# Kernel tuning notes

Measured on AMD Instinct MI355X. Metric: run time of the kernel, lower is better.

The kernel has to match this reference:

```python
import jax, jax.numpy as jnp
import numpy as np

B, N, D, H = 2, 1024, 512, 16
DH = D // H  # d_head = 32
NEG_INF = -1e9
LN_EPS = 1e-5


def setup_inputs() -> dict:
    key = jax.random.key(0)
    ks = jax.random.split(key, 12)
    x = jax.random.normal(ks[0], (B, N, D), dtype=jnp.float32)
    pdist = jax.random.uniform(ks[1], (B, N, N), dtype=jnp.float32)
    angle = jax.random.normal(ks[2], (B, N, N, 2), dtype=jnp.float32)
    adj = jax.random.uniform(ks[3], (B, N, N), dtype=jnp.float32)
    mask = jnp.zeros((B, 1, 1, N), dtype=bool)
    # parameters
    gamma_p = jnp.ones((H,), dtype=jnp.float32)
    gamma_adj = jnp.ones((H,), dtype=jnp.float32)
    w_bias = jax.random.normal(ks[4], (H, 2), dtype=jnp.float32) / np.sqrt(2.0)   # Linear(2,H).weight
    att_w = jax.random.normal(ks[5], (3 * H * DH, D), dtype=jnp.float32) / np.sqrt(D)  # Linear(D,3HDh).weight
    ff_w = jax.random.normal(ks[6], (D, H * DH), dtype=jnp.float32) / np.sqrt(H * DH)  # Linear(HDh,D).weight
    ff_b = jnp.zeros((D,), dtype=jnp.float32)
    ln_w = jnp.ones((D,), dtype=jnp.float32)
    ln_b = jnp.zeros((D,), dtype=jnp.float32)
    return dict(x=x, pdist=pdist, angle=angle, adj=adj, mask=mask,
                gamma_p=gamma_p, gamma_adj=gamma_adj, w_bias=w_bias,
                att_w=att_w, ff_w=ff_w, ff_b=ff_b, ln_w=ln_w, ln_b=ln_b)


def reference(x, pdist, angle, adj, mask, gamma_p, gamma_adj, w_bias,
              att_w, ff_w, ff_b, ln_w, ln_b):
    bsz, n_atoms, _ = x.shape
    # QKV projection
    qkv = x @ att_w.T                              # [B,N,3*H*DH]
    wq, wk, wv = jnp.split(qkv, 3, axis=-1)
    wq = wq.reshape(bsz, n_atoms, H, DH)
    wk = wk.reshape(bsz, n_atoms, H, DH)
    wv = wv.reshape(bsz, n_atoms, H, DH)
    # scores with additive biases
    score = jnp.einsum('bihd,bjhd->bhij', wq, wk) / jnp.sqrt(jnp.float32(DH))
    score = score - gamma_p[None, :, None, None] * pdist[:, None]
    angle_bias = jnp.einsum('bijc,hc->bhij', angle, w_bias)
    score = score + angle_bias
    score = score + gamma_adj[None, :, None, None] * adj[:, None]
    score = jnp.where(mask, NEG_INF, score)
    prob = jax.nn.softmax(score, axis=-1)          # [B,H,N,N]
    att_vec = jnp.einsum('bhij,bjhd->bihd', prob, wv).reshape(bsz, n_atoms, H * DH)
    ff_out = att_vec @ ff_w.T + ff_b               # [B,N,D]
    y = x + ff_out
    mu = jnp.mean(y, axis=-1, keepdims=True)
    var = jnp.mean(jnp.square(y - mu), axis=-1, keepdims=True)
    return (y - mu) / jnp.sqrt(var + LN_EPS) * ln_w + ln_b
```

## Files before the change

### kernel.cpp

```cpp
#include <hip/hip_runtime.h>
#include <hip/hip_bf16.h>
#include <stdint.h>

#define DEVI __device__ __forceinline__

typedef __attribute__((ext_vector_type(4))) float f32x4;
typedef __attribute__((ext_vector_type(16))) float f32x16;
typedef __attribute__((ext_vector_type(8))) short bf16x8;

constexpr int nB = 2, nN = 1024, nD = 512, nH = 16, nDH = 32;

DEVI unsigned short f2bf(float x) {
  unsigned u = __float_as_uint(x);
  return (unsigned short)((u + 0x7fffu + ((u >> 16) & 1u)) >> 16);
}
DEVI float bf2f(unsigned short s) { return __uint_as_float(((unsigned)s) << 16); }
DEVI unsigned pk2(float lo, float hi_) {
  return (unsigned)f2bf(lo) | ((unsigned)f2bf(hi_) << 16);
}
DEVI float bperm(int srclane, float v) {
  return __int_as_float(__builtin_amdgcn_ds_bpermute(srclane << 2, __float_as_int(v)));
}
DEVI void gload16(const void* g, void* l) {
  __builtin_amdgcn_global_load_lds((const __attribute__((address_space(1))) void*)g,
                                   (__attribute__((address_space(3))) void*)l, 16, 0, 0);
}

__global__ __launch_bounds__(256) void cvt_kernel(const float* __restrict__ x,
                                                  const float* __restrict__ aw,
                                                  const float* __restrict__ fw,
                                                  unsigned short* __restrict__ xb,
                                                  unsigned short* __restrict__ awb,
                                                  unsigned short* __restrict__ fwb) {
  int i = blockIdx.x * 256 + threadIdx.x;
  const float* src; unsigned short* dst; int base;
  if (i < 262144)      { src = x;  dst = xb;  base = i; }
  else if (i < 458752) { src = aw; dst = awb; base = i - 262144; }
  else                 { src = fw; dst = fwb; base = i - 458752; }
  float4 v = reinterpret_cast<const float4*>(src)[base];
  ushort4 o;
  o.x = f2bf(v.x); o.y = f2bf(v.y); o.z = f2bf(v.z); o.w = f2bf(v.w);
  reinterpret_cast<ushort4*>(dst)[base] = o;
}

template <int BM, int BN, int MODE>
__global__ __launch_bounds__(256, 4) void gemm_bt(const unsigned short* __restrict__ A,
                                                  const unsigned short* __restrict__ Bw,
                                                  unsigned short* __restrict__ q,
                                                  unsigned short* __restrict__ kmat,
                                                  unsigned short* __restrict__ vm,
                                                  float* __restrict__ C,
                                                  int K, int Ncols) {
  constexpr int MW = BM / 2, NW = BN / 2;
  constexpr int MF = MW / 16, NF = NW / 16;
  constexpr int IA = BM / 16, IB = BN / 16, PW = (IA + IB) / 4;
  __shared__ __align__(16) unsigned short sA[2][BM * 32];
  __shared__ __align__(16) unsigned short sB[2][BN * 32];
  const int tid = threadIdx.x, wid = tid >> 6, lane = tid & 63;
  const int wr = wid >> 1, wc = wid & 1;
  const long rowA = (long)blockIdx.x * BM;
  const long rowB = (long)blockIdx.y * BN;
  const int srow = lane >> 2, scol = (lane & 3) * 8;

  f32x4 acc[MF][NF];
#pragma unroll
  for (int mm = 0; mm < MF; ++mm)
#pragma unroll
    for (int nn = 0; nn < NF; ++nn)
#pragma unroll
      for (int r = 0; r < 4; ++r) acc[mm][nn][r] = 0.f;

  auto stage = [&](int t, int pb) {
    const int k0 = t * 32;
#pragma unroll
    for (int j = 0; j < PW; ++j) {
      int g = wid + 4 * j;
      if (g < IA) {
        gload16(&A[(rowA + g * 16 + srow) * K + k0 + scol], &sA[pb][g * 512]);
      } else {
        int c = g - IA;
        gload16(&Bw[(rowB + c * 16 + srow) * K + k0 + scol], &sB[pb][c * 512]);
      }
    }
  };
  auto comp = [&](int pb) {
    const int kg = (lane >> 4) * 8, rlo = lane & 15;
    bf16x8 af[MF], bfv[NF];
#pragma unroll
    for (int mm = 0; mm < MF; ++mm)
      af[mm] = *reinterpret_cast<const bf16x8*>(&sA[pb][(MW * wr + 16 * mm + rlo) * 32 + kg]);
#pragma unroll
    for (int nn = 0; nn < NF; ++nn)
      bfv[nn] = *reinterpret_cast<const bf16x8*>(&sB[pb][(NW * wc + 16 * nn + rlo) * 32 + kg]);
#pragma unroll
    for (int mm = 0; mm < MF; ++mm)
#pragma unroll
      for (int nn = 0; nn < NF; ++nn)
        acc[mm][nn] = __builtin_amdgcn_mfma_f32_16x16x32_bf16(af[mm], bfv[nn],
                                                              acc[mm][nn], 0, 0, 0);
  };

  const int NT = K / 32;
  stage(0, 0);
  __syncthreads();
  for (int t = 0; t < NT; t += 2) {
    if (t + 1 < NT) stage(t + 1, 1);
    comp(0);
    __syncthreads();
    if (t + 2 < NT) stage(t + 2, 0);
    if (t + 1 < NT) comp(1);
    __syncthreads();
  }

#pragma unroll
  for (int mm = 0; mm < MF; ++mm)
#pragma unroll
    for (int nn = 0; nn < NF; ++nn)
#pragma unroll
      for (int r = 0; r < 4; ++r) {
        float v = acc[mm][nn][r];
        int row = (int)rowA + MW * wr + 16 * mm + (lane >> 4) * 4 + r;
        int col = (int)rowB + NW * wc + 16 * nn + (lane & 15);
        if constexpr (MODE == 0) {
          int s = col >> 9, rem = col & 511;
          int h = rem >> 5, d = rem & 31;
          int b = row >> 10, n = row & 1023;
          long idx = ((long)(b * nH + h) * nN + n) * nDH + d;
          if (s == 0)      q[idx]    = f2bf(v * 0.1767766952966369f);
          else if (s == 1) kmat[idx] = f2bf(v);
          else             vm[idx]   = f2bf(v);
        } else {
          C[(long)row * Ncols + col] = v;
        }
      }
}

__global__ __launch_bounds__(256) void vtrans_kernel(const unsigned short* __restrict__ vm,
                                                     unsigned short* __restrict__ vtt) {
  const int g = blockIdx.x, bh = g >> 3, oct = g & 7;
  const int t = threadIdx.x;
  __shared__ unsigned short tile[32][36];
  for (int s = 0; s < 4; ++s) {
    const int jt = oct * 4 + s;
    {
      int r = t >> 3, c4 = (t & 7) * 4;
      *reinterpret_cast<ushort4*>(&tile[r][c4]) = *reinterpret_cast<const ushort4*>(
          vm + ((long)bh * nN + jt * 32 + r) * 32 + c4);
    }
    __syncthreads();
    {
      int d = t >> 3, j4 = (t & 7) * 4;
      ushort4 o;
      o.x = tile[j4][d]; o.y = tile[j4 + 1][d];
      o.z = tile[j4 + 2][d]; o.w = tile[j4 + 3][d];
      *reinterpret_cast<ushort4*>(vtt + ((long)bh * 32 + jt) * 1024 + d * 32 + j4) = o;
    }
    __syncthreads();
  }
}

__global__ __launch_bounds__(1024, 4) void attn_kernel(
    const unsigned short* __restrict__ qm, const unsigned short* __restrict__ km,
    const unsigned short* __restrict__ vtt,
    const float* __restrict__ pdist, const float* __restrict__ angle,
    const float* __restrict__ adj, const unsigned char* __restrict__ mask,
    const float* __restrict__ gamma_p, const float* __restrict__ gamma_adj,
    const float* __restrict__ w_bias,
    unsigned short* __restrict__ po, float* __restrict__ pm, float* __restrict__ pl) {
  const int b = blockIdx.x >> 5, it = blockIdx.x & 31;
  const int jc = blockIdx.y;
  const int tid = threadIdx.x, wid = tid >> 6, lane = tid & 63;
  const int h = wid;
  const int li = lane & 31, hi = lane >> 5;
  const int ibase = it * 32;

  __shared__ __align__(16) float s_pd[2][1024], s_adj[2][1024];
  __shared__ __align__(16) float s_a0[2][1024], s_a1[2][1024];
  __shared__ __align__(16) float s_mk[1024];

  const float gp = gamma_p[h], ga = gamma_adj[h];
  const float wb0 = w_bias[2 * h], wb1 = w_bias[2 * h + 1];

  const unsigned short* qb = qm + ((long)(b * nH + h) * nN + ibase) * nDH;
  const bf16x8 qf0 = *reinterpret_cast<const bf16x8*>(qb + li * 32 + hi * 8);
  const bf16x8 qf1 = *reinterpret_cast<const bf16x8*>(qb + li * 32 + 16 + hi * 8);

  f32x16 o;
#pragma unroll
  for (int r = 0; r < 16; ++r) o[r] = 0.f;
  float mrun = -INFINITY, lrun = 0.f;

  auto stage = [&](int s, int pb) {
    const int jbase = (jc * 8 + s) * 32;
    if (tid < 512) {
      int r = (tid >> 3) & 31, c = tid & 7;
      const float* src = (tid < 256 ? pdist : adj) +
                         ((long)b * nN + ibase + r) * nN + jbase + c * 4;
      float4 v = *reinterpret_cast<const float4*>(src);
      float* dst = (tid < 256 ? s_pd[pb] : s_adj[pb]) + r * 32 + ((c ^ (r & 7)) << 2);
      *reinterpret_cast<float4*>(dst) = v;
    } else {
      int t2 = tid - 512;
      int r = t2 >> 4, p = t2 & 15;
      float4 v = *reinterpret_cast<const float4*>(
          angle + (((long)b * nN + ibase + r) * nN + jbase + p * 2) * 2);
      int off = r * 32 + (((p >> 1) ^ (r & 7)) << 2) + (p & 1) * 2;
      *reinterpret_cast<float2*>(s_a0[pb] + off) = make_float2(v.x, v.z);
      *reinterpret_cast<float2*>(s_a1[pb] + off) = make_float2(v.y, v.w);
    }
  };

  auto comp = [&](int s, int pb) {
    const int jt = jc * 8 + s, jbase = jt * 32;
    const unsigned short* kb = km + ((long)(b * nH + h) * nN + jbase) * nDH;
    bf16x8 kf0 = *reinterpret_cast<const bf16x8*>(kb + li * 32 + hi * 8);
    bf16x8 kf1 = *reinterpret_cast<const bf16x8*>(kb + li * 32 + 16 + hi * 8);
    f32x16 sc;
#pragma unroll
    for (int r = 0; r < 16; ++r) sc[r] = 0.f;
    sc = __builtin_amdgcn_mfma_f32_32x32x16_bf16(kf0, qf0, sc, 0, 0, 0);
    sc = __builtin_amdgcn_mfma_f32_32x32x16_bf16(kf1, qf1, sc, 0, 0, 0);

    float sv[16];
    float tmax = -INFINITY;
#pragma unroll
    for (int g = 0; g < 4; ++g) {
      const int cs = (((2 * g + hi) ^ (li & 7)) << 2);
      f32x4 pdq = *reinterpret_cast<const f32x4*>(s_pd[pb] + li * 32 + cs);
      f32x4 adq = *reinterpret_cast<const f32x4*>(s_adj[pb] + li * 32 + cs);
      f32x4 a0q = *reinterpret_cast<const f32x4*>(s_a0[pb] + li * 32 + cs);
      f32x4 a1q = *reinterpret_cast<const f32x4*>(s_a1[pb] + li * 32 + cs);
      f32x4 mkq = *reinterpret_cast<const f32x4*>(s_mk + jbase + 8 * g + 4 * hi);
#pragma unroll
      for (int u = 0; u < 4; ++u) {
        float x = sc[4 * g + u] - gp * pdq[u] + wb0 * a0q[u] + wb1 * a1q[u]
                  + ga * adq[u] + mkq[u];
        sv[4 * g + u] = x;
        tmax = fmaxf(tmax, x);
      }
    }
    tmax = fmaxf(tmax, __shfl_xor(tmax, 32));
    if (__any((int)(tmax > mrun + 8.f))) {
      float mnew = fmaxf(mrun, tmax);
      float alpha = __expf(mrun - mnew);
      lrun *= alpha;
#pragma unroll
      for (int r = 0; r < 16; ++r) o[r] *= bperm((r & 3) + 8 * (r >> 2) + 4 * hi, alpha);
      mrun = mnew;
    }
    float psum = 0.f;
#pragma unroll
    for (int r = 0; r < 16; ++r) { sv[r] = __expf(sv[r] - mrun); psum += sv[r]; }
    psum += __shfl_xor(psum, 32);
    lrun += psum;

    unsigned ow[8], rw[8];
#pragma unroll
    for (int t = 0; t < 8; ++t) ow[t] = pk2(sv[2 * t], sv[2 * t + 1]);
#pragma unroll
    for (int t = 0; t < 8; ++t) rw[t] = __shfl_xor(ow[t], 32);
    union U { unsigned u[4]; bf16x8 v; };
    U u0, u1;
    if (hi == 0) {
      u0.u[0] = ow[0]; u0.u[1] = ow[1]; u0.u[2] = rw[0]; u0.u[3] = rw[1];
      u1.u[0] = ow[4]; u1.u[1] = ow[5]; u1.u[2] = rw[4]; u1.u[3] = rw[5];
    } else {
      u0.u[0] = rw[2]; u0.u[1] = rw[3]; u0.u[2] = ow[2]; u0.u[3] = ow[3];
      u1.u[0] = rw[6]; u1.u[1] = rw[7]; u1.u[2] = ow[6]; u1.u[3] = ow[7];
    }

    const unsigned short* vb = vtt + ((long)(b * nH + h) * 32 + jt) * 1024;
    bf16x8 vf0 = *reinterpret_cast<const bf16x8*>(vb + li * 32 + hi * 8);
    bf16x8 vf1 = *reinterpret_cast<const bf16x8*>(vb + li * 32 + 16 + hi * 8);
    o = __builtin_amdgcn_mfma_f32_32x32x16_bf16(u0.v, vf0, o, 0, 0, 0);
    o = __builtin_amdgcn_mfma_f32_32x32x16_bf16(u1.v, vf1, o, 0, 0, 0);
  };

  s_mk[tid] = mask[b * nN + tid] ? -1e9f : 0.f;
  stage(0, 0);
  __syncthreads();
  for (int s = 0; s < 8; s += 2) {
    if (s + 1 < 8) stage(s + 1, 1);
    comp(s, 0);
    __syncthreads();
    if (s + 2 < 8) stage(s + 2, 0);
    comp(s + 1, 1);
    __syncthreads();
  }

  const long task = (((long)(b * nH + h) * 32 + it) * 4 + jc);
  unsigned short* pob = po + task * 1024;
#pragma unroll
  for (int r = 0; r < 16; ++r) {
    const int irow = (r & 3) + 8 * (r >> 2) + 4 * hi;
    pob[irow * 32 + li] = f2bf(o[r]);
  }
  if (hi == 0) { pm[task * 32 + li] = mrun; pl[task * 32 + li] = lrun; }
}

__global__ __launch_bounds__(256) void merge_kernel(const unsigned short* __restrict__ po,
                                                    const float* __restrict__ pm,
                                                    const float* __restrict__ pl,
                                                    unsigned short* __restrict__ attb) {
  const int x = blockIdx.x;
  const int t = threadIdx.x;
  const int i = t >> 3, d4 = (t & 7) * 4;
  const long tb = (long)x * 4;
  float m[4], l[4];
#pragma unroll
  for (int c = 0; c < 4; ++c) { m[c] = pm[(tb + c) * 32 + i]; l[c] = pl[(tb + c) * 32 + i]; }
  float M = fmaxf(fmaxf(m[0], m[1]), fmaxf(m[2], m[3]));
  float L = 0.f, w[4];
#pragma unroll
  for (int c = 0; c < 4; ++c) { w[c] = __expf(m[c] - M); L += w[c] * l[c]; }
  float o0 = 0, o1 = 0, o2 = 0, o3 = 0;
#pragma unroll
  for (int c = 0; c < 4; ++c) {
    ushort4 v = *reinterpret_cast<const ushort4*>(po + (tb + c) * 1024 + i * 32 + d4);
    o0 += w[c] * bf2f(v.x); o1 += w[c] * bf2f(v.y);
    o2 += w[c] * bf2f(v.z); o3 += w[c] * bf2f(v.w);
  }
  const float inv = 1.f / L;
  const int b = x >> 9, hh = (x >> 5) & 15, it = x & 31;
  ushort4 ov;
  ov.x = f2bf(o0 * inv); ov.y = f2bf(o1 * inv);
  ov.z = f2bf(o2 * inv); ov.w = f2bf(o3 * inv);
  *reinterpret_cast<ushort4*>(attb + ((long)b * nN + it * 32 + i) * nD + hh * 32 + d4) = ov;
}

__global__ __launch_bounds__(256) void ln_kernel(const float* __restrict__ x,
                                                 const float* __restrict__ ffc,
                                                 const float* __restrict__ ffb,
                                                 const float* __restrict__ lnw,
                                                 const float* __restrict__ lnb,
                                                 float* __restrict__ out) {
  const int row = blockIdx.x, tid = threadIdx.x;
  const int wid = tid >> 6, lane = tid & 63;
  const int c = tid * 2;
  const long base = (long)row * nD + c;
  float2 xv = *reinterpret_cast<const float2*>(x + base);
  float2 cv = *reinterpret_cast<const float2*>(ffc + base);
  float2 bv = *reinterpret_cast<const float2*>(ffb + c);
  float y0 = xv.x + cv.x + bv.x, y1 = xv.y + cv.y + bv.y;
  float s = y0 + y1, s2 = y0 * y0 + y1 * y1;
#pragma unroll
  for (int off = 1; off < 64; off <<= 1) {
    s += __shfl_xor(s, off);
    s2 += __shfl_xor(s2, off);
  }
  __shared__ float red[8];
  if (lane == 0) { red[wid] = s; red[4 + wid] = s2; }
  __syncthreads();
  s = red[0] + red[1] + red[2] + red[3];
  s2 = red[4] + red[5] + red[6] + red[7];
  const float mu = s * (1.f / nD);
  const float var = s2 * (1.f / nD) - mu * mu;
  const float rs = rsqrtf(var + 1e-5f);
  float2 wv = *reinterpret_cast<const float2*>(lnw + c);
  float2 lv = *reinterpret_cast<const float2*>(lnb + c);
  float2 ov;
  ov.x = (y0 - mu) * rs * wv.x + lv.x;
  ov.y = (y1 - mu) * rs * wv.y + lv.y;
  *reinterpret_cast<float2*>(out + base) = ov;
}

extern "C" void kernel_launch(void* const* d_in, const int* in_sizes, int n_in,
                              void* d_out, int out_size, void* d_ws, size_t ws_size,
                              hipStream_t stream) {
  const float* x         = (const float*)d_in[0];
  const float* pdist     = (const float*)d_in[1];
  const float* angle     = (const float*)d_in[2];
  const float* adj       = (const float*)d_in[3];
  const unsigned char* mask = (const unsigned char*)d_in[4];
  const float* gamma_p   = (const float*)d_in[5];
  const float* gamma_adj = (const float*)d_in[6];
  const float* w_bias    = (const float*)d_in[7];
  const float* att_w     = (const float*)d_in[8];
  const float* ff_w      = (const float*)d_in[9];
  const float* ff_b      = (const float*)d_in[10];
  const float* ln_w      = (const float*)d_in[11];
  const float* ln_b      = (const float*)d_in[12];
  float* out = (float*)d_out;

  char* ws = (char*)d_ws;
  float*          ffc  = (float*)(ws);
  unsigned short* xb   = (unsigned short*)(ws + 0x400000);
  unsigned short* vm   = (unsigned short*)(ws + 0x600000);
  unsigned short* awb  = (unsigned short*)(ws + 0x800000);
  unsigned short* fwb  = (unsigned short*)(ws + 0x980000);
  unsigned short* qm   = (unsigned short*)(ws + 0xA00000);
  unsigned short* km   = (unsigned short*)(ws + 0xC00000);
  unsigned short* vtt  = (unsigned short*)(ws + 0xE00000);
  unsigned short* po   = (unsigned short*)(ws);
  float*          pm   = (float*)(ws + 0x800000);
  float*          pl   = (float*)(ws + 0x880000);
  unsigned short* attb = km;

  hipLaunchKernelGGL(cvt_kernel, dim3(2048), dim3(256), 0, stream,
                     x, att_w, ff_w, xb, awb, fwb);
  hipLaunchKernelGGL((gemm_bt<64, 128, 0>), dim3(32, 12), dim3(256), 0, stream,
                     xb, awb, qm, km, vm, nullptr, 512, 0);
  hipLaunchKernelGGL(vtrans_kernel, dim3(256), dim3(256), 0, stream, vm, vtt);
  hipLaunchKernelGGL(attn_kernel, dim3(64, 4), dim3(1024), 0, stream,
                     qm, km, vtt, pdist, angle, adj, mask,
                     gamma_p, gamma_adj, w_bias, po, pm, pl);
  hipLaunchKernelGGL(merge_kernel, dim3(1024), dim3(256), 0, stream,
                     po, pm, pl, attb);
  hipLaunchKernelGGL((gemm_bt<64, 64, 1>), dim3(32, 8), dim3(256), 0, stream,
                     attb, fwb, nullptr, nullptr, nullptr, ffc, 512, 512);
  hipLaunchKernelGGL(ln_kernel, dim3(2048), dim3(256), 0, stream,
                     x, ffc, ff_b, ln_w, ln_b, out);
}
```

Baseline: 162.7 us.

## Fuse bf16 conversion, V transpose, split merge, and FF+LayerNorm into fewer kernels

Converts fp32 inputs to bf16 inside the QKV GEMM staging and writes V directly in transposed tile layout, removing the separate convert and transpose kernels. The split-softmax merge now runs in the attention kernel: the last block per row tile, found with an atomic counter, does the merge. The output projection is fused with the residual add and LayerNorm in one kernel of 32-row tiles covering all 512 columns. This cuts launch count and intermediate round trips, but the FF kernel uses only 64 blocks and re-reads and converts the full fp32 weight in each block.

```diff
diff --git a/kernel.cpp b/kernel.cpp
--- a/kernel.cpp
+++ b/kernel.cpp
@@ -26,137 +26,102 @@
                                    (__attribute__((address_space(3))) void*)l, 16, 0, 0);
 }
 
-__global__ __launch_bounds__(256) void cvt_kernel(const float* __restrict__ x,
-                                                  const float* __restrict__ aw,
-                                                  const float* __restrict__ fw,
-                                                  unsigned short* __restrict__ xb,
-                                                  unsigned short* __restrict__ awb,
-                                                  unsigned short* __restrict__ fwb) {
-  int i = blockIdx.x * 256 + threadIdx.x;
-  const float* src; unsigned short* dst; int base;
-  if (i < 262144)      { src = x;  dst = xb;  base = i; }
-  else if (i < 458752) { src = aw; dst = awb; base = i - 262144; }
-  else                 { src = fw; dst = fwb; base = i - 458752; }
-  float4 v = reinterpret_cast<const float4*>(src)[base];
-  ushort4 o;
-  o.x = f2bf(v.x); o.y = f2bf(v.y); o.z = f2bf(v.z); o.w = f2bf(v.w);
-  reinterpret_cast<ushort4*>(dst)[base] = o;
-}
-
-template <int BM, int BN, int MODE>
-__global__ __launch_bounds__(256, 4) void gemm_bt(const unsigned short* __restrict__ A,
-                                                  const unsigned short* __restrict__ Bw,
-                                                  unsigned short* __restrict__ q,
-                                                  unsigned short* __restrict__ kmat,
-                                                  unsigned short* __restrict__ vm,
-                                                  float* __restrict__ C,
-                                                  int K, int Ncols) {
-  constexpr int MW = BM / 2, NW = BN / 2;
-  constexpr int MF = MW / 16, NF = NW / 16;
-  constexpr int IA = BM / 16, IB = BN / 16, PW = (IA + IB) / 4;
-  __shared__ __align__(16) unsigned short sA[2][BM * 32];
-  __shared__ __align__(16) unsigned short sB[2][BN * 32];
+__global__ __launch_bounds__(256, 2) void qkv_gemm(const float* __restrict__ x,
+                                                   const float* __restrict__ aw,
+                                                   unsigned short* __restrict__ q,
+                                                   unsigned short* __restrict__ kmat,
+                                                   unsigned short* __restrict__ vtt) {
+  __shared__ __align__(16) unsigned short sA[2][64 * 32];
+  __shared__ __align__(16) unsigned short sB[2][128 * 32];
   const int tid = threadIdx.x, wid = tid >> 6, lane = tid & 63;
   const int wr = wid >> 1, wc = wid & 1;
-  const long rowA = (long)blockIdx.x * BM;
-  const long rowB = (long)blockIdx.y * BN;
-  const int srow = lane >> 2, scol = (lane & 3) * 8;
-
-  f32x4 acc[MF][NF];
-#pragma unroll
-  for (int mm = 0; mm < MF; ++mm)
-#pragma unroll
-    for (int nn = 0; nn < NF; ++nn)
+  const long rowA = (long)blockIdx.x * 64;
+  const long rowB = (long)blockIdx.y * 128;
+
+  f32x4 acc[2][4];
+#pragma unroll
+  for (int mm = 0; mm < 2; ++mm)
+#pragma unroll
+    for (int nn = 0; nn < 4; ++nn)
 #pragma unroll
       for (int r = 0; r < 4; ++r) acc[mm][nn][r] = 0.f;
+
+  union PK { unsigned u[4]; bf16x8 v; };
 
   auto stage = [&](int t, int pb) {
     const int k0 = t * 32;
-#pragma unroll
-    for (int j = 0; j < PW; ++j) {
-      int g = wid + 4 * j;
-      if (g < IA) {
-        gload16(&A[(rowA + g * 16 + srow) * K + k0 + scol], &sA[pb][g * 512]);
-      } else {
-        int c = g - IA;
-        gload16(&Bw[(rowB + c * 16 + srow) * K + k0 + scol], &sB[pb][c * 512]);
-      }
+    {
+      const float* src = x + (rowA + (tid >> 2)) * 512 + k0 + (tid & 3) * 8;
+      float4 v0 = *reinterpret_cast<const float4*>(src);
+      float4 v1 = *reinterpret_cast<const float4*>(src + 4);
+      PK p;
+      p.u[0] = pk2(v0.x, v0.y); p.u[1] = pk2(v0.z, v0.w);
+      p.u[2] = pk2(v1.x, v1.y); p.u[3] = pk2(v1.z, v1.w);
+      *reinterpret_cast<bf16x8*>(&sA[pb][tid * 8]) = p.v;
+    }
+    {
+      const float* src = aw + (rowB + (tid >> 1)) * 512 + k0 + (tid & 1) * 16;
+      float4 w0 = *reinterpret_cast<const float4*>(src);
+      float4 w1 = *reinterpret_cast<const float4*>(src + 4);
+      float4 w2 = *reinterpret_cast<const float4*>(src + 8);
+      float4 w3 = *reinterpret_cast<const float4*>(src + 12);
+      PK p0, p1;
+      p0.u[0] = pk2(w0.x, w0.y); p0.u[1] = pk2(w0.z, w0.w);
+      p0.u[2] = pk2(w1.x, w1.y); p0.u[3] = pk2(w1.z, w1.w);
+      p1.u[0] = pk2(w2.x, w2.y); p1.u[1] = pk2(w2.z, w2.w);
+      p1.u[2] = pk2(w3.x, w3.y); p1.u[3] = pk2(w3.z, w3.w);
+      *reinterpret_cast<bf16x8*>(&sB[pb][tid * 16]) = p0.v;
+      *reinterpret_cast<bf16x8*>(&sB[pb][tid * 16 + 8]) = p1.v;
     }
   };
   auto comp = [&](int pb) {
     const int kg = (lane >> 4) * 8, rlo = lane & 15;
-    bf16x8 af[MF], bfv[NF];
-#pragma unroll
-    for (int mm = 0; mm < MF; ++mm)
-      af[mm] = *reinterpret_cast<const bf16x8*>(&sA[pb][(MW * wr + 16 * mm + rlo) * 32 + kg]);
-#pragma unroll
-    for (int nn = 0; nn < NF; ++nn)
-      bfv[nn] = *reinterpret_cast<const bf16x8*>(&sB[pb][(NW * wc + 16 * nn + rlo) * 32 + kg]);
-#pragma unroll
-    for (int mm = 0; mm < MF; ++mm)
-#pragma unroll
-      for (int nn = 0; nn < NF; ++nn)
+    bf16x8 af[2], bfv[4];
+#pragma unroll
+    for (int mm = 0; mm < 2; ++mm)
+      af[mm] = *reinterpret_cast<const bf16x8*>(&sA[pb][(32 * wr + 16 * mm + rlo) * 32 + kg]);
+#pragma unroll
+    for (int nn = 0; nn < 4; ++nn)
+      bfv[nn] = *reinterpret_cast<const bf16x8*>(&sB[pb][(64 * wc + 16 * nn + rlo) * 32 + kg]);
+#pragma unroll
+    for (int mm = 0; mm < 2; ++mm)
+#pragma unroll
+      for (int nn = 0; nn < 4; ++nn)
         acc[mm][nn] = __builtin_amdgcn_mfma_f32_16x16x32_bf16(af[mm], bfv[nn],
                                                               acc[mm][nn], 0, 0, 0);
   };
 
-  const int NT = K / 32;
   stage(0, 0);
   __syncthreads();
-  for (int t = 0; t < NT; t += 2) {
-    if (t + 1 < NT) stage(t + 1, 1);
+  for (int t = 0; t < 16; t += 2) {
+    if (t + 1 < 16) stage(t + 1, 1);
     comp(0);
     __syncthreads();
-    if (t + 2 < NT) stage(t + 2, 0);
-    if (t + 1 < NT) comp(1);
-    __syncthreads();
-  }
-
-#pragma unroll
-  for (int mm = 0; mm < MF; ++mm)
-#pragma unroll
-    for (int nn = 0; nn < NF; ++nn)
+    if (t + 2 < 16) stage(t + 2, 0);
+    comp(1);
+    __syncthreads();
+  }
+
+#pragma unroll
+  for (int mm = 0; mm < 2; ++mm)
+#pragma unroll
+    for (int nn = 0; nn < 4; ++nn)
 #pragma unroll
       for (int r = 0; r < 4; ++r) {
         float v = acc[mm][nn][r];
-        int row = (int)rowA + MW * wr + 16 * mm + (lane >> 4) * 4 + r;
-        int col = (int)rowB + NW * wc + 16 * nn + (lane & 15);
-        if constexpr (MODE == 0) {
-          int s = col >> 9, rem = col & 511;
-          int h = rem >> 5, d = rem & 31;
-          int b = row >> 10, n = row & 1023;
-          long idx = ((long)(b * nH + h) * nN + n) * nDH + d;
-          if (s == 0)      q[idx]    = f2bf(v * 0.1767766952966369f);
-          else if (s == 1) kmat[idx] = f2bf(v);
-          else             vm[idx]   = f2bf(v);
+        int row = (int)rowA + 32 * wr + 16 * mm + (lane >> 4) * 4 + r;
+        int col = (int)rowB + 64 * wc + 16 * nn + (lane & 15);
+        int s = col >> 9, rem = col & 511;
+        int h = rem >> 5, d = rem & 31;
+        int b = row >> 10, n = row & 1023;
+        if (s == 0) {
+          q[((long)(b * nH + h) * nN + n) * nDH + d] = f2bf(v * 0.1767766952966369f);
+        } else if (s == 1) {
+          kmat[((long)(b * nH + h) * nN + n) * nDH + d] = f2bf(v);
         } else {
-          C[(long)row * Ncols + col] = v;
+          vtt[((long)(b * nH + h) * 32 + (n >> 5)) * 1024 + d * 32 + (n & 31)] = f2bf(v);
         }
       }
-}
-
-__global__ __launch_bounds__(256) void vtrans_kernel(const unsigned short* __restrict__ vm,
-                                                     unsigned short* __restrict__ vtt) {
-  const int g = blockIdx.x, bh = g >> 3, oct = g & 7;
-  const int t = threadIdx.x;
-  __shared__ unsigned short tile[32][36];
-  for (int s = 0; s < 4; ++s) {
-    const int jt = oct * 4 + s;
-    {
-      int r = t >> 3, c4 = (t & 7) * 4;
-      *reinterpret_cast<ushort4*>(&tile[r][c4]) = *reinterpret_cast<const ushort4*>(
-          vm + ((long)bh * nN + jt * 32 + r) * 32 + c4);
-    }
-    __syncthreads();
-    {
-      int d = t >> 3, j4 = (t & 7) * 4;
-      ushort4 o;
-      o.x = tile[j4][d]; o.y = tile[j4 + 1][d];
-      o.z = tile[j4 + 2][d]; o.w = tile[j4 + 3][d];
-      *reinterpret_cast<ushort4*>(vtt + ((long)bh * 32 + jt) * 1024 + d * 32 + j4) = o;
-    }
-    __syncthreads();
-  }
 }
 
 __global__ __launch_bounds__(1024, 4) void attn_kernel(
@@ -166,7 +131,8 @@
     const float* __restrict__ adj, const unsigned char* __restrict__ mask,
     const float* __restrict__ gamma_p, const float* __restrict__ gamma_adj,
     const float* __restrict__ w_bias,
-    unsigned short* __restrict__ po, float* __restrict__ pm, float* __restrict__ pl) {
+    unsigned short* __restrict__ po, float* __restrict__ pm, float* __restrict__ pl,
+    int* __restrict__ cnt, unsigned short* __restrict__ attb) {
   const int b = blockIdx.x >> 5, it = blockIdx.x & 31;
   const int jc = blockIdx.y;
   const int tid = threadIdx.x, wid = tid >> 6, lane = tid & 63;
@@ -177,6 +143,7 @@
   __shared__ __align__(16) float s_pd[2][1024], s_adj[2][1024];
   __shared__ __align__(16) float s_a0[2][1024], s_a1[2][1024];
   __shared__ __align__(16) float s_mk[1024];
+  __shared__ int s_last;
 
   const float gp = gamma_p[h], ga = gamma_adj[h];
   const float wb0 = w_bias[2 * h], wb1 = w_bias[2 * h + 1];
@@ -233,10 +200,10 @@
       f32x4 mkq = *reinterpret_cast<const f32x4*>(s_mk + jbase + 8 * g + 4 * hi);
 #pragma unroll
       for (int u = 0; u < 4; ++u) {
-        float x = sc[4 * g + u] - gp * pdq[u] + wb0 * a0q[u] + wb1 * a1q[u]
-                  + ga * adq[u] + mkq[u];
-        sv[4 * g + u] = x;
-        tmax = fmaxf(tmax, x);
+        float xv = sc[4 * g + u] - gp * pdq[u] + wb0 * a0q[u] + wb1 * a1q[u]
+                   + ga * adq[u] + mkq[u];
+        sv[4 * g + u] = xv;
+        tmax = fmaxf(tmax, xv);
       }
     }
     tmax = fmaxf(tmax, __shfl_xor(tmax, 32));
@@ -296,72 +263,151 @@
     pob[irow * 32 + li] = f2bf(o[r]);
   }
   if (hi == 0) { pm[task * 32 + li] = mrun; pl[task * 32 + li] = lrun; }
-}
-
-__global__ __launch_bounds__(256) void merge_kernel(const unsigned short* __restrict__ po,
-                                                    const float* __restrict__ pm,
-                                                    const float* __restrict__ pl,
-                                                    unsigned short* __restrict__ attb) {
-  const int x = blockIdx.x;
-  const int t = threadIdx.x;
-  const int i = t >> 3, d4 = (t & 7) * 4;
-  const long tb = (long)x * 4;
-  float m[4], l[4];
-#pragma unroll
-  for (int c = 0; c < 4; ++c) { m[c] = pm[(tb + c) * 32 + i]; l[c] = pl[(tb + c) * 32 + i]; }
-  float M = fmaxf(fmaxf(m[0], m[1]), fmaxf(m[2], m[3]));
-  float L = 0.f, w[4];
-#pragma unroll
-  for (int c = 0; c < 4; ++c) { w[c] = __expf(m[c] - M); L += w[c] * l[c]; }
-  float o0 = 0, o1 = 0, o2 = 0, o3 = 0;
-#pragma unroll
-  for (int c = 0; c < 4; ++c) {
-    ushort4 v = *reinterpret_cast<const ushort4*>(po + (tb + c) * 1024 + i * 32 + d4);
-    o0 += w[c] * bf2f(v.x); o1 += w[c] * bf2f(v.y);
-    o2 += w[c] * bf2f(v.z); o3 += w[c] * bf2f(v.w);
-  }
-  const float inv = 1.f / L;
-  const int b = x >> 9, hh = (x >> 5) & 15, it = x & 31;
-  ushort4 ov;
-  ov.x = f2bf(o0 * inv); ov.y = f2bf(o1 * inv);
-  ov.z = f2bf(o2 * inv); ov.w = f2bf(o3 * inv);
-  *reinterpret_cast<ushort4*>(attb + ((long)b * nN + it * 32 + i) * nD + hh * 32 + d4) = ov;
-}
-
-__global__ __launch_bounds__(256) void ln_kernel(const float* __restrict__ x,
-                                                 const float* __restrict__ ffc,
-                                                 const float* __restrict__ ffb,
-                                                 const float* __restrict__ lnw,
-                                                 const float* __restrict__ lnb,
-                                                 float* __restrict__ out) {
-  const int row = blockIdx.x, tid = threadIdx.x;
-  const int wid = tid >> 6, lane = tid & 63;
-  const int c = tid * 2;
-  const long base = (long)row * nD + c;
-  float2 xv = *reinterpret_cast<const float2*>(x + base);
-  float2 cv = *reinterpret_cast<const float2*>(ffc + base);
-  float2 bv = *reinterpret_cast<const float2*>(ffb + c);
-  float y0 = xv.x + cv.x + bv.x, y1 = xv.y + cv.y + bv.y;
-  float s = y0 + y1, s2 = y0 * y0 + y1 * y1;
-#pragma unroll
-  for (int off = 1; off < 64; off <<= 1) {
-    s += __shfl_xor(s, off);
-    s2 += __shfl_xor(s2, off);
-  }
-  __shared__ float red[8];
-  if (lane == 0) { red[wid] = s; red[4 + wid] = s2; }
-  __syncthreads();
-  s = red[0] + red[1] + red[2] + red[3];
-  s2 = red[4] + red[5] + red[6] + red[7];
-  const float mu = s * (1.f / nD);
-  const float var = s2 * (1.f / nD) - mu * mu;
-  const float rs = rsqrtf(var + 1e-5f);
-  float2 wv = *reinterpret_cast<const float2*>(lnw + c);
-  float2 lv = *reinterpret_cast<const float2*>(lnb + c);
-  float2 ov;
-  ov.x = (y0 - mu) * rs * wv.x + lv.x;
-  ov.y = (y1 - mu) * rs * wv.y + lv.y;
-  *reinterpret_cast<float2*>(out + base) = ov;
+
+  __syncthreads();
+  if (tid == 0) {
+    __threadfence();
+    int old = atomicAdd(&cnt[b * 32 + it], 1);
+    s_last = (old == 3);
+  }
+  __syncthreads();
+  if (s_last) {
+    __threadfence();
+    const long tb = (((long)(b * nH + h) * 32 + it) * 4);
+#pragma unroll
+    for (int s = 0; s < 4; ++s) {
+      const int t64 = lane + 64 * s;
+      const int i = t64 >> 3, d4 = (t64 & 7) * 4;
+      float m[4], l[4];
+#pragma unroll
+      for (int c = 0; c < 4; ++c) {
+        m[c] = pm[(tb + c) * 32 + i];
+        l[c] = pl[(tb + c) * 32 + i];
+      }
+      float M = fmaxf(fmaxf(m[0], m[1]), fmaxf(m[2], m[3]));
+      float L = 0.f, w[4];
+#pragma unroll
+      for (int c = 0; c < 4; ++c) { w[c] = __expf(m[c] - M); L += w[c] * l[c]; }
+      float o0 = 0, o1 = 0, o2 = 0, o3 = 0;
+#pragma unroll
+      for (int c = 0; c < 4; ++c) {
+        ushort4 v = *reinterpret_cast<const ushort4*>(po + (tb + c) * 1024 + i * 32 + d4);
+        o0 += w[c] * bf2f(v.x); o1 += w[c] * bf2f(v.y);
+        o2 += w[c] * bf2f(v.z); o3 += w[c] * bf2f(v.w);
+      }
+      const float inv = 1.f / L;
+      ushort4 ov;
+      ov.x = f2bf(o0 * inv); ov.y = f2bf(o1 * inv);
+      ov.z = f2bf(o2 * inv); ov.w = f2bf(o3 * inv);
+      *reinterpret_cast<ushort4*>(attb + ((long)b * nN + it * 32 + i) * nD + h * 32 + d4) = ov;
+    }
+  }
+}
+
+__global__ __launch_bounds__(512, 2) void ffln_kernel(const unsigned short* __restrict__ attb,
+                                                      const float* __restrict__ fw,
+                                                      const float* __restrict__ x,
+                                                      const float* __restrict__ ffb,
+                                                      const float* __restrict__ lnw,
+                                                      const float* __restrict__ lnb,
+                                                      float* __restrict__ out) {
+  __shared__ __align__(16) unsigned short sA[2][32 * 32];
+  __shared__ __align__(16) unsigned short sB[2][512 * 32];
+  __shared__ float rs_[32][4], rs2_[32][4];
+  const int tid = threadIdx.x, wid = tid >> 6, lane = tid & 63;
+  const int wr = wid >> 2, wc = wid & 3;
+  const long rowA = (long)blockIdx.x * 32;
+
+  f32x4 acc[8];
+#pragma unroll
+  for (int nn = 0; nn < 8; ++nn)
+#pragma unroll
+    for (int r = 0; r < 4; ++r) acc[nn][r] = 0.f;
+
+  auto stage = [&](int t, int pb) {
+    const int k0 = t * 32;
+    if (tid < 128)
+      gload16(&attb[(rowA + (tid >> 2)) * 512 + k0 + (tid & 3) * 8], &sA[pb][tid * 8]);
+    const int row_r = tid >> 3, kq = (tid & 7) * 4;
+#pragma unroll
+    for (int c = 0; c < 8; ++c) {
+      float4 v = *reinterpret_cast<const float4*>(fw + (row_r + 64 * c) * 512 + k0 + kq);
+      unsigned p0 = pk2(v.x, v.y), p1 = pk2(v.z, v.w);
+      uint2 pw; pw.x = p0; pw.y = p1;
+      *reinterpret_cast<uint2*>(&sB[pb][(row_r + 64 * c) * 32 + kq]) = pw;
+    }
+  };
+  auto comp = [&](int pb) {
+    const int kg = (lane >> 4) * 8, rlo = lane & 15;
+    bf16x8 af = *reinterpret_cast<const bf16x8*>(&sA[pb][(16 * wr + rlo) * 32 + kg]);
+#pragma unroll
+    for (int nn = 0; nn < 8; ++nn) {
+      bf16x8 bfv = *reinterpret_cast<const bf16x8*>(&sB[pb][(128 * wc + 16 * nn + rlo) * 32 + kg]);
+      acc[nn] = __builtin_amdgcn_mfma_f32_16x16x32_bf16(af, bfv, acc[nn], 0, 0, 0);
+    }
+  };
+
+  stage(0, 0);
+  __syncthreads();
+  for (int t = 0; t < 16; t += 2) {
+    if (t + 1 < 16) stage(t + 1, 1);
+    comp(0);
+    __syncthreads();
+    if (t + 2 < 16) stage(t + 2, 0);
+    comp(1);
+    __syncthreads();
+  }
+
+  float colf[8], colw[8], colb[8];
+#pragma unroll
+  for (int nn = 0; nn < 8; ++nn) {
+    int c = 128 * wc + 16 * nn + (lane & 15);
+    colf[nn] = ffb[c]; colw[nn] = lnw[c]; colb[nn] = lnb[c];
+  }
+  float s[4], s2[4];
+#pragma unroll
+  for (int r = 0; r < 4; ++r) { s[r] = 0.f; s2[r] = 0.f; }
+#pragma unroll
+  for (int nn = 0; nn < 8; ++nn)
+#pragma unroll
+    for (int r = 0; r < 4; ++r) {
+      long row = rowA + 16 * wr + 4 * (lane >> 4) + r;
+      int c = 128 * wc + 16 * nn + (lane & 15);
+      float y = acc[nn][r] + colf[nn] + x[row * 512 + c];
+      acc[nn][r] = y;
+      s[r] += y; s2[r] += y * y;
+    }
+#pragma unroll
+  for (int off = 1; off < 16; off <<= 1)
+#pragma unroll
+    for (int r = 0; r < 4; ++r) {
+      s[r] += __shfl_xor(s[r], off);
+      s2[r] += __shfl_xor(s2[r], off);
+    }
+  if ((lane & 15) == 0) {
+#pragma unroll
+    for (int r = 0; r < 4; ++r) {
+      int rowl = 16 * wr + 4 * (lane >> 4) + r;
+      rs_[rowl][wc] = s[r];
+      rs2_[rowl][wc] = s2[r];
+    }
+  }
+  __syncthreads();
+#pragma unroll
+  for (int r = 0; r < 4; ++r) {
+    int rowl = 16 * wr + 4 * (lane >> 4) + r;
+    float S = rs_[rowl][0] + rs_[rowl][1] + rs_[rowl][2] + rs_[rowl][3];
+    float S2 = rs2_[rowl][0] + rs2_[rowl][1] + rs2_[rowl][2] + rs2_[rowl][3];
+    float mu = S * (1.f / 512.f);
+    float var = S2 * (1.f / 512.f) - mu * mu;
+    float rstd = rsqrtf(var + 1e-5f);
+    long row = rowA + rowl;
+#pragma unroll
+    for (int nn = 0; nn < 8; ++nn) {
+      int c = 128 * wc + 16 * nn + (lane & 15);
+      out[row * 512 + c] = (acc[nn][r] - mu) * rstd * colw[nn] + colb[nn];
+    }
+  }
 }
 
 extern "C" void kernel_launch(void* const* d_in, const int* in_sizes, int n_in,
@@ -383,31 +429,21 @@
   float* out = (float*)d_out;
 
   char* ws = (char*)d_ws;
-  float*          ffc  = (float*)(ws);
-  unsigned short* xb   = (unsigned short*)(ws + 0x400000);
-  unsigned short* vm   = (unsigned short*)(ws + 0x600000);
-  unsigned short* awb  = (unsigned short*)(ws + 0x800000);
-  unsigned short* fwb  = (unsigned short*)(ws + 0x980000);
-  unsigned short* qm   = (unsigned short*)(ws + 0xA00000);
-  unsigned short* km   = (unsigned short*)(ws + 0xC00000);
-  unsigned short* vtt  = (unsigned short*)(ws + 0xE00000);
-  unsigned short* po   = (unsigned short*)(ws);
-  float*          pm   = (float*)(ws + 0x800000);
-  float*          pl   = (float*)(ws + 0x880000);
-  unsigned short* attb = km;
-
-  hipLaunchKernelGGL(cvt_kernel, dim3(2048), dim3(256), 0, stream,
-                     x, att_w, ff_w, xb, awb, fwb);
-  hipLaunchKernelGGL((gemm_bt<64, 128, 0>), dim3(32, 12), dim3(256), 0, stream,
-                     xb, awb, qm, km, vm, nullptr, 512, 0);
-  hipLaunchKernelGGL(vtrans_kernel, dim3(256), dim3(256), 0, stream, vm, vtt);
+  unsigned short* qm   = (unsigned short*)(ws);
+  unsigned short* km   = (unsigned short*)(ws + 0x200000);
+  unsigned short* vtt  = (unsigned short*)(ws + 0x400000);
+  unsigned short* po   = (unsigned short*)(ws + 0x600000);
+  float*          pm   = (float*)(ws + 0xE00000);
+  float*          pl   = (float*)(ws + 0xE80000);
+  int*            cnt  = (int*)(ws + 0xF00000);
+  unsigned short* attb = (unsigned short*)(ws + 0x1000000);
+
+  hipMemsetAsync(cnt, 0, 64 * sizeof(int), stream);
+  hipLaunchKernelGGL(qkv_gemm, dim3(32, 12), dim3(256), 0, stream,
+                     x, att_w, qm, km, vtt);
   hipLaunchKernelGGL(attn_kernel, dim3(64, 4), dim3(1024), 0, stream,
                      qm, km, vtt, pdist, angle, adj, mask,
-                     gamma_p, gamma_adj, w_bias, po, pm, pl);
-  hipLaunchKernelGGL(merge_kernel, dim3(1024), dim3(256), 0, stream,
-                     po, pm, pl, attb);
-  hipLaunchKernelGGL((gemm_bt<64, 64, 1>), dim3(32, 8), dim3(256), 0, stream,
-                     attb, fwb, nullptr, nullptr, nullptr, ffc, 512, 512);
-  hipLaunchKernelGGL(ln_kernel, dim3(2048), dim3(256), 0, stream,
-                     x, ffc, ff_b, ln_w, ln_b, out);
-}
+                     gamma_p, gamma_adj, w_bias, po, pm, pl, cnt, attb);
+  hipLaunchKernelGGL(ffln_kernel, dim3(64), dim3(512), 0, stream,
+                     attb, ff_w, x, ff_b, ln_w, ln_b, out);
+}
```

New measurement: 207.9 us. 1.28x slower.
